# Performance work log

Hardware: AMD Instinct MI355X
Metric: run time of the kernel (lower is better)

## Reference

```python
import jax, jax.numpy as jnp
import numpy as np

P, U, B, C, S = 200000, 100000, 5000, 2000, 1000
N = P + U + B + C + S
E_PB, E_PC, E_PS, E_UP = 200000, 200000, 400000, 1000000


def setup_inputs() -> dict:
    key = jax.random.key(0)
    ks = jax.random.split(key, 21)
    d = {
        'product_x': jax.random.normal(ks[0], (P, 384), jnp.float32),
        'user_emb': jax.random.normal(ks[1], (U, 64), jnp.float32),
        'brand_emb': jax.random.normal(ks[2], (B, 64), jnp.float32),
        'cat_emb': jax.random.normal(ks[3], (C, 64), jnp.float32),
        'shop_emb': jax.random.normal(ks[4], (S, 64), jnp.float32),
        'proj_W': jax.random.normal(ks[5], (384, 64), jnp.float32) * 0.05,
        'proj_b': jax.random.normal(ks[6], (64,), jnp.float32) * 0.05,
        'c1_Wl': jax.random.normal(ks[7], (64, 64), jnp.float32) * 0.1,
        'c1_bl': jax.random.normal(ks[8], (64,), jnp.float32) * 0.1,
        'c1_Wr': jax.random.normal(ks[9], (64, 64), jnp.float32) * 0.1,
        'c2_Wl': jax.random.normal(ks[10], (64, 32), jnp.float32) * 0.1,
        'c2_bl': jax.random.normal(ks[11], (32,), jnp.float32) * 0.1,
        'c2_Wr': jax.random.normal(ks[12], (64, 32), jnp.float32) * 0.1,
        'pb_src': jax.random.randint(ks[13], (E_PB,), 0, P, jnp.int32),
        'pb_dst': jax.random.randint(ks[14], (E_PB,), 0, B, jnp.int32),
        'pc_src': jax.random.randint(ks[15], (E_PC,), 0, P, jnp.int32),
        'pc_dst': jax.random.randint(ks[16], (E_PC,), 0, C, jnp.int32),
        'ps_src': jax.random.randint(ks[17], (E_PS,), 0, P, jnp.int32),
        'ps_dst': jax.random.randint(ks[18], (E_PS,), 0, S, jnp.int32),
        'up_src': jax.random.randint(ks[19], (E_UP,), 0, U, jnp.int32),
        'up_dst': jax.random.randint(ks[20], (E_UP,), 0, P, jnp.int32),
    }
    return d


def _combined_edges(pb_src, pb_dst, pc_src, pc_dst, ps_src, ps_dst, up_src, up_dst):
    # global node id offsets: [product | user | brand | category | shop]
    off_u, off_b, off_c, off_s = P, P + U, P + U + B, P + U + B + C
    pb_d = pb_dst + off_b
    pc_d = pc_dst + off_c
    ps_d = ps_dst + off_s
    up_s = up_src + off_u
    src = jnp.concatenate([pb_src, pb_d, pc_src, pc_d, ps_src, ps_d, up_s, up_dst])
    dst = jnp.concatenate([pb_d, pb_src, pc_d, pc_src, ps_d, ps_src, up_dst, up_s])
    return src, dst


def _sage_conv(x, src, dst, Wl, bl, Wr):
    # PyG SAGEConv (mean aggr): out = lin_l(mean_{j in N(i)} x_j) + lin_r(x_i)
    msg = x[src]  # [E, d] gather
    ssum = jax.ops.segment_sum(msg, dst, num_segments=N)
    cnt = jax.ops.segment_sum(jnp.ones((src.shape[0],), x.dtype), dst, num_segments=N)
    aggr = ssum / jnp.maximum(cnt, 1.0)[:, None]
    return aggr @ Wl + bl + x @ Wr


def reference(product_x, user_emb, brand_emb, cat_emb, shop_emb,
              proj_W, proj_b, c1_Wl, c1_bl, c1_Wr, c2_Wl, c2_bl, c2_Wr,
              pb_src, pb_dst, pc_src, pc_dst, ps_src, ps_dst, up_src, up_dst):
    prod_h = jax.nn.relu(product_x @ proj_W + proj_b)
    x = jnp.concatenate([prod_h, user_emb, brand_emb, cat_emb, shop_emb], axis=0)  # [N, 64]
    src, dst = _combined_edges(pb_src, pb_dst, pc_src, pc_dst, ps_src, ps_dst, up_src, up_dst)
    x = jax.nn.relu(_sage_conv(x, src, dst, c1_Wl, c1_bl, c1_Wr))
    # dropout(p=0.2) is identity in eval mode
    x = _sage_conv(x, src, dst, c2_Wl, c2_bl, c2_Wr)  # [N, 32]
    # output_dict is just contiguous slices of x: product/user/brand/category/shop
    return x
```

## Files before the change

kernel.cpp:

```cpp
#include <hip/hip_runtime.h>

#define NP 200000
#define NU 100000
#define NBR 5000
#define NCAT 2000
#define NSH 1000
#define NN (NP + NU + NBR + NCAT + NSH)
#define OFF_U NP
#define OFF_B (NP + NU)
#define OFF_C (NP + NU + NBR)
#define OFF_S (NP + NU + NBR + NCAT)

#define NBINS 67

typedef unsigned short u16;
typedef unsigned int u32;
typedef __attribute__((ext_vector_type(8))) short short8;
typedef __attribute__((ext_vector_type(4))) float f32x4;

__device__ __forceinline__ u16 f2bf(float f) {
  union { float f; unsigned u; } v;
  v.f = f;
  unsigned r = (v.u + 0x7fffu + ((v.u >> 16) & 1u)) >> 16;
  return (u16)r;
}
__device__ __forceinline__ float uasf(u32 u) {
  union { u32 u; float f; } v;
  v.u = u;
  return v.f;
}
__device__ __forceinline__ u32 cvtpk(float lo, float hi) {
  u32 r;
  asm("v_cvt_pk_bf16_f32 %0, %1, %2" : "=v"(r) : "v"(lo), "v"(hi));
  return r;
}

__device__ __forceinline__ int bin_of(int a) {
  if (a < OFF_U) return a >> 13;
  if (a < OFF_B) return 25 + ((a - OFF_U) >> 13);
  if (a < OFF_C) return 38 + ((a - OFF_B) >> 10);
  if (a < OFF_S) return 43 + ((a - OFF_C) >> 8);
  return 51 + ((a - OFF_S) >> 6);
}
__device__ __forceinline__ void bin_range(int bin, int& n0, int& n1) {
  if (bin < 25) {
    n0 = bin << 13; n1 = min(n0 + 8192, OFF_U);
  } else if (bin < 38) {
    n0 = OFF_U + ((bin - 25) << 13); n1 = min(n0 + 8192, OFF_B);
  } else if (bin < 43) {
    n0 = OFF_B + ((bin - 38) << 10); n1 = min(n0 + 1024, OFF_C);
  } else if (bin < 51) {
    n0 = OFF_C + ((bin - 43) << 8); n1 = min(n0 + 256, OFF_S);
  } else {
    n0 = OFF_S + ((bin - 51) << 6); n1 = min(n0 + 64, NN);
  }
}

__global__ __launch_bounds__(256) void proj_mfma_kernel(
    const float* __restrict__ px, const float* __restrict__ W,
    const float* __restrict__ bias, u16* __restrict__ xb) {
  __shared__ u16 lA[2][128 * 32];
  const int t = threadIdx.x;
  const int l = t & 63;
  const int wid = t >> 6;
  const int row0 = blockIdx.x * 128;

  const int n0 = wid * 16 + (l & 15);
  const int kb = (l >> 4) * 8;
  short8 bf[12];
#pragma unroll
  for (int kt = 0; kt < 12; ++kt) {
    union { u32 p[4]; short8 s; } uu;
#pragma unroll
    for (int j = 0; j < 4; ++j) {
      const float lo = W[(size_t)(kt * 32 + kb + 2 * j) * 64 + n0];
      const float hi = W[(size_t)(kt * 32 + kb + 2 * j + 1) * 64 + n0];
      uu.p[j] = cvtpk(lo, hi);
    }
    bf[kt] = uu.s;
  }
  const float bv = bias[n0];

  f32x4 acc[8];
#pragma unroll
  for (int rt = 0; rt < 8; ++rt) {
    f32x4 z = {0.f, 0.f, 0.f, 0.f};
    acc[rt] = z;
  }

  const int fr_base = (((l & 15) * 64 + (l >> 4) * 16)) ^ ((l & 7) << 4);

  float4 sreg[4];
#pragma unroll
  for (int i = 0; i < 4; ++i) {
    const int qi = t + 256 * i;
    const int r = qi >> 3, q = qi & 7;
    const int grow = row0 + r;
    sreg[i] = (grow < NP) ? *reinterpret_cast<const float4*>(px + (size_t)grow * 384 + q * 4)
                          : make_float4(0.f, 0.f, 0.f, 0.f);
  }
#pragma unroll
  for (int i = 0; i < 4; ++i) {
    const int qi = t + 256 * i;
    const int r = qi >> 3, q = qi & 7;
    const int a16 = (((r * 64 + q * 8)) ^ ((r & 7) << 4)) >> 1;
    const u32 p0 = cvtpk(sreg[i].x, sreg[i].y);
    const u32 p1 = cvtpk(sreg[i].z, sreg[i].w);
    *reinterpret_cast<uint2*>(&lA[0][a16]) = make_uint2(p0, p1);
  }

#pragma unroll
  for (int kt = 0; kt < 12; ++kt) {
    const int cur = kt & 1;
    if (kt + 1 < 12) {
#pragma unroll
      for (int i = 0; i < 4; ++i) {
        const int qi = t + 256 * i;
        const int r = qi >> 3, q = qi & 7;
        const int grow = row0 + r;
        sreg[i] = (grow < NP)
                      ? *reinterpret_cast<const float4*>(px + (size_t)grow * 384 +
                                                         (kt + 1) * 32 + q * 4)
                      : make_float4(0.f, 0.f, 0.f, 0.f);
      }
    }
    __syncthreads();
#pragma unroll
    for (int rt = 0; rt < 8; ++rt) {
      const short8 af =
          *reinterpret_cast<const short8*>(&lA[cur][(fr_base + rt * 1024) >> 1]);
      acc[rt] = __builtin_amdgcn_mfma_f32_16x16x32_bf16(af, bf[kt], acc[rt], 0, 0, 0);
    }
    if (kt + 1 < 12) {
#pragma unroll
      for (int i = 0; i < 4; ++i) {
        const int qi = t + 256 * i;
        const int r = qi >> 3, q = qi & 7;
        const int a16 = (((r * 64 + q * 8)) ^ ((r & 7) << 4)) >> 1;
        const u32 p0 = cvtpk(sreg[i].x, sreg[i].y);
        const u32 p1 = cvtpk(sreg[i].z, sreg[i].w);
        *reinterpret_cast<uint2*>(&lA[cur ^ 1][a16]) = make_uint2(p0, p1);
      }
    }
  }

#pragma unroll
  for (int rt = 0; rt < 8; ++rt) {
#pragma unroll
    for (int r = 0; r < 4; ++r) {
      const int grow = row0 + rt * 16 + (l >> 4) * 4 + r;
      if (grow < NP)
        xb[(size_t)grow * 64 + n0] = f2bf(fmaxf(acc[rt][r] + bv, 0.f));
    }
  }
}

__global__ void cvt_emb_kernel(const float* __restrict__ ue, const float* __restrict__ be,
                               const float* __restrict__ ce, const float* __restrict__ se,
                               u16* __restrict__ xb) {
  const int i = blockIdx.x * 256 + threadIdx.x;
  const int totalQ = (NU + NBR + NCAT + NSH) * 16;
  if (i >= totalQ) return;
  const int row = i >> 4, q = i & 15;
  const float* src;
  int lrow;
  if (row < NU) {
    src = ue; lrow = row;
  } else if (row < NU + NBR) {
    src = be; lrow = row - NU;
  } else if (row < NU + NBR + NCAT) {
    src = ce; lrow = row - NU - NBR;
  } else {
    src = se; lrow = row - NU - NBR - NCAT;
  }
  const float4 v = reinterpret_cast<const float4*>(src)[(size_t)lrow * 16 + q];
  ushort4 o;
  o.x = f2bf(v.x);
  o.y = f2bf(v.y);
  o.z = f2bf(v.z);
  o.w = f2bf(v.w);
  reinterpret_cast<ushort4*>(xb + (size_t)(OFF_U + row) * 64)[q] = o;
}

__device__ __forceinline__ void decode_edge(
    int i, const int* pbs, const int* pbd, const int* pcs, const int* pcd,
    const int* pss, const int* psd, const int* ups, const int* upd,
    int nPB, int nPC, int nPS, int& a, int& b) {
  const int d = i & 1;
  int eu = i >> 1;
  int a0, b0;
  if (eu < nPB) {
    a0 = pbs[eu]; b0 = pbd[eu] + OFF_B;
  } else {
    eu -= nPB;
    if (eu < nPC) {
      a0 = pcs[eu]; b0 = pcd[eu] + OFF_C;
    } else {
      eu -= nPC;
      if (eu < nPS) {
        a0 = pss[eu]; b0 = psd[eu] + OFF_S;
      } else {
        eu -= nPS;
        a0 = ups[eu] + OFF_U; b0 = upd[eu];
      }
    }
  }
  a = d ? b0 : a0;
  b = d ? a0 : b0;
}

#define EDGE_ARGS const int* __restrict__ pbs, const int* __restrict__ pbd, \
                  const int* __restrict__ pcs, const int* __restrict__ pcd, \
                  const int* __restrict__ pss, const int* __restrict__ psd, \
                  const int* __restrict__ ups, const int* __restrict__ upd, \
                  int nPB, int nPC, int nPS, int nD
#define EDGE_PASS pbs, pbd, pcs, pcd, pss, psd, ups, upd, nPB, nPC, nPS

__global__ __launch_bounds__(256) void bin_count_kernel(EDGE_ARGS,
                                                        int* __restrict__ binCnt) {
  __shared__ int lh[NBINS];
  const int t = threadIdx.x;
  if (t < NBINS) lh[t] = 0;
  __syncthreads();
  for (int i = blockIdx.x * 256 + t; i < nD; i += gridDim.x * 256) {
    int a, b;
    decode_edge(i, EDGE_PASS, a, b);
    (void)b;
    atomicAdd(&lh[bin_of(a)], 1);
  }
  __syncthreads();
  if (t < NBINS && lh[t] > 0) atomicAdd(&binCnt[t], lh[t]);
}

__global__ void bin_scan_kernel(const int* __restrict__ binCnt, int* __restrict__ binBase,
                                int* __restrict__ gcur) {
  __shared__ int base[NBINS + 1];
  if (threadIdx.x == 0) {
    int run = 0;
    for (int b = 0; b < NBINS; ++b) {
      base[b] = run;
      run += binCnt[b];
    }
    base[NBINS] = run;
  }
  __syncthreads();
  if (threadIdx.x <= NBINS) binBase[threadIdx.x] = base[threadIdx.x];
  if (threadIdx.x < NBINS) gcur[threadIdx.x * 16] = base[threadIdx.x];
}

__global__ __launch_bounds__(256) void bin_scatter_kernel(EDGE_ARGS,
                                                          uint2* __restrict__ gbuf,
                                                          int* __restrict__ gcur) {
  __shared__ int lh[NBINS];
  __shared__ int gb[NBINS];
  __shared__ int ofs[NBINS];
  const int t = threadIdx.x;
  const int per = (nD + gridDim.x - 1) / gridDim.x;
  const int start = blockIdx.x * per;
  const int end = (start + per < nD) ? (start + per) : nD;

  if (t < NBINS) {
    lh[t] = 0;
    ofs[t] = 0;
  }
  __syncthreads();
  for (int i = start + t; i < end; i += 256) {
    int a, b;
    decode_edge(i, EDGE_PASS, a, b);
    (void)b;
    atomicAdd(&lh[bin_of(a)], 1);
  }
  __syncthreads();
  if (t < NBINS && lh[t] > 0) gb[t] = atomicAdd(&gcur[t * 16], lh[t]);
  __syncthreads();
  for (int i = start + t; i < end; i += 256) {
    int a, b;
    decode_edge(i, EDGE_PASS, a, b);
    const int bb = bin_of(a);
    const int d = atomicAdd(&ofs[bb], 1);
    gbuf[gb[bb] + d] = make_uint2((u32)a, (u32)b);
  }
}

__global__ __launch_bounds__(256) void count_nodes_kernel(
    const uint2* __restrict__ gbuf, const int* __restrict__ binBase,
    int* __restrict__ cntp) {
  __shared__ int cnt[8192];
  const int bin = blockIdx.x >> 2, s = blockIdx.x & 3;
  int n0, n1;
  bin_range(bin, n0, n1);
  const int rb = binBase[bin], re = binBase[bin + 1];
  const int len = re - rb;
  const int s0 = rb + (len * s) / 4;
  const int s1 = rb + (len * (s + 1)) / 4;
  for (int i = threadIdx.x; i < 8192; i += 256) cnt[i] = 0;
  __syncthreads();
  for (int r = s0 + threadIdx.x; r < s1; r += 256)
    atomicAdd(&cnt[(int)gbuf[r].x - n0], 1);
  __syncthreads();
  for (int n = n0 + threadIdx.x; n < n1; n += 256)
    cntp[s * NN + n] = cnt[n - n0];
}

__global__ __launch_bounds__(256) void scan1_kernel(const int* __restrict__ cntp,
                                                    int* __restrict__ blockSums, int n) {
  __shared__ int sdata[256];
  const int base = blockIdx.x * 1024;
  int s = 0;
  for (int i = threadIdx.x; i < 1024; i += 256) {
    int idx = base + i;
    if (idx < n)
      s += cntp[idx] + cntp[NN + idx] + cntp[2 * NN + idx] + cntp[3 * NN + idx];
  }
  sdata[threadIdx.x] = s;
  __syncthreads();
  for (int off = 128; off > 0; off >>= 1) {
    if (threadIdx.x < off) sdata[threadIdx.x] += sdata[threadIdx.x + off];
    __syncthreads();
  }
  if (threadIdx.x == 0) blockSums[blockIdx.x] = sdata[0];
}

__global__ __launch_bounds__(512) void scan2_kernel(int* __restrict__ blockSums, int nb) {
  __shared__ int sd[512];
  const int t = threadIdx.x;
  const int v = (t < nb) ? blockSums[t] : 0;
  sd[t] = v;
  __syncthreads();
  for (int off = 1; off < 512; off <<= 1) {
    int add = (t >= off) ? sd[t - off] : 0;
    __syncthreads();
    sd[t] += add;
    __syncthreads();
  }
  if (t < nb) blockSums[t] = sd[t] - v;
}

__global__ __launch_bounds__(256) void scan3_kernel(const int* __restrict__ cntp,
                                                    const int* __restrict__ blockSums,
                                                    int* __restrict__ rowptr, int n) {
  __shared__ int wsum[4];
  const int base = blockIdx.x * 1024;
  const int t = threadIdx.x, lane = t & 63, wid = t >> 6;
  const int idx0 = base + t * 4;
  int v[4];
#pragma unroll
  for (int j = 0; j < 4; ++j) {
    int idx = idx0 + j;
    v[j] = (idx < n)
               ? cntp[idx] + cntp[NN + idx] + cntp[2 * NN + idx] + cntp[3 * NN + idx]
               : 0;
  }
  const int s = v[0] + v[1] + v[2] + v[3];
  int incl = s;
  for (int off = 1; off < 64; off <<= 1) {
    int tt = __shfl_up(incl, off);
    if (lane >= off) incl += tt;
  }
  if (lane == 63) wsum[wid] = incl;
  __syncthreads();
  int wOff = 0;
#pragma unroll
  for (int w = 0; w < 4; ++w)
    if (w < wid) wOff += wsum[w];
  int run = blockSums[blockIdx.x] + wOff + (incl - s);
#pragma unroll
  for (int j = 0; j < 4; ++j) {
    int idx = idx0 + j;
    if (idx < n) {
      rowptr[idx] = run;
      run += v[j];
      if (idx == n - 1) rowptr[n] = run;
    }
  }
}

__global__ __launch_bounds__(256) void fill_scatter_kernel(
    const uint2* __restrict__ gbuf, const int* __restrict__ binBase,
    const int* __restrict__ rowptr, const int* __restrict__ cntp,
    int* __restrict__ eidx) {
  __shared__ int cur[8192];
  const int bin = blockIdx.x >> 2, s = blockIdx.x & 3;
  int n0, n1;
  bin_range(bin, n0, n1);
  const int rb = binBase[bin], re = binBase[bin + 1];
  const int len = re - rb;
  const int s0 = rb + (len * s) / 4;
  const int s1 = rb + (len * (s + 1)) / 4;
  for (int n = n0 + threadIdx.x; n < n1; n += 256) {
    int c = rowptr[n];
    if (s > 0) c += cntp[n];
    if (s > 1) c += cntp[NN + n];
    if (s > 2) c += cntp[2 * NN + n];
    cur[n - n0] = c;
  }
  __syncthreads();
  for (int r = s0 + threadIdx.x; r < s1; r += 256) {
    const uint2 rec = gbuf[r];
    const int p = atomicAdd(&cur[(int)rec.x - n0], 1);
    eidx[p] = (int)rec.y;
  }
}

__global__ __launch_bounds__(256) void gather_mean_kernel(
    const int* __restrict__ rowptr, const int* __restrict__ eidx,
    const uint4* __restrict__ xin, uint4* __restrict__ sout) {
  const int lane = threadIdx.x & 63;
  const int q = lane & 7;
  const int h = lane >> 3;
  const int wid0 = blockIdx.x * 4 + (threadIdx.x >> 6);
  const int nW = gridDim.x * 4;
  for (int node = wid0; node < NN; node += nW) {
    const int r0 = rowptr[node], r1 = rowptr[node + 1];
    float s0 = 0.f, s1 = 0.f, s2 = 0.f, s3 = 0.f, s4 = 0.f, s5 = 0.f, s6 = 0.f,
          s7 = 0.f;
    for (int e = r0; e < r1; e += 16) {
      const int ee0 = e + h;
      const int ee1 = e + 8 + h;
      uint4 va = make_uint4(0u, 0u, 0u, 0u);
      uint4 vb = make_uint4(0u, 0u, 0u, 0u);
      if (ee0 < r1) va = xin[(size_t)eidx[ee0] * 8 + q];
      if (ee1 < r1) vb = xin[(size_t)eidx[ee1] * 8 + q];
      s0 += uasf(va.x << 16) + uasf(vb.x << 16);
      s1 += uasf(va.x & 0xffff0000u) + uasf(vb.x & 0xffff0000u);
      s2 += uasf(va.y << 16) + uasf(vb.y << 16);
      s3 += uasf(va.y & 0xffff0000u) + uasf(vb.y & 0xffff0000u);
      s4 += uasf(va.z << 16) + uasf(vb.z << 16);
      s5 += uasf(va.z & 0xffff0000u) + uasf(vb.z & 0xffff0000u);
      s6 += uasf(va.w << 16) + uasf(vb.w << 16);
      s7 += uasf(va.w & 0xffff0000u) + uasf(vb.w & 0xffff0000u);
    }
#pragma unroll
    for (int off = 8; off < 64; off <<= 1) {
      s0 += __shfl_xor(s0, off);
      s1 += __shfl_xor(s1, off);
      s2 += __shfl_xor(s2, off);
      s3 += __shfl_xor(s3, off);
      s4 += __shfl_xor(s4, off);
      s5 += __shfl_xor(s5, off);
      s6 += __shfl_xor(s6, off);
      s7 += __shfl_xor(s7, off);
    }
    if (h == 0) {
      const int deg = r1 - r0;
      const float inv = (deg > 0) ? (1.f / (float)deg) : 1.f;
      uint4 o;
      o.x = cvtpk(s0 * inv, s1 * inv);
      o.y = cvtpk(s2 * inv, s3 * inv);
      o.z = cvtpk(s4 * inv, s5 * inv);
      o.w = cvtpk(s6 * inv, s7 * inv);
      sout[(size_t)node * 8 + q] = o;
    }
  }
}

template <int DOUT, bool RELU>
__global__ __launch_bounds__(256) void layer_gemm_kernel(
    const u32* __restrict__ S, const u32* __restrict__ X,
    const float* __restrict__ Wl, const float* __restrict__ bl,
    const float* __restrict__ Wr, void* __restrict__ outv) {
  constexpr int NC = DOUT / 4;
  constexpr int NR = 256 / NC;
  constexpr int R = 128 / NR;
  __shared__ __align__(16) u32 lS[128 * 32];
  __shared__ __align__(16) u32 lX[128 * 32];
  __shared__ __align__(16) float lWl[64 * DOUT];
  __shared__ __align__(16) float lWr[64 * DOUT];
  const int t = threadIdx.x;
  const int row0 = blockIdx.x * 128;

#pragma unroll
  for (int i = 0; i < (64 * DOUT) / 1024; ++i) {
    const int idx = i * 256 + t;
    reinterpret_cast<float4*>(lWl)[idx] = reinterpret_cast<const float4*>(Wl)[idx];
    reinterpret_cast<float4*>(lWr)[idx] = reinterpret_cast<const float4*>(Wr)[idx];
  }
#pragma unroll
  for (int i = 0; i < 4; ++i) {
    const int idx = i * 256 + t;
    const int r = idx >> 3, c = idx & 7;
    uint4 vs = make_uint4(0u, 0u, 0u, 0u), vx = vs;
    if (row0 + r < NN) {
      vs = reinterpret_cast<const uint4*>(S)[(size_t)(row0 + r) * 8 + c];
      vx = reinterpret_cast<const uint4*>(X)[(size_t)(row0 + r) * 8 + c];
    }
    reinterpret_cast<uint4*>(lS)[idx] = vs;
    reinterpret_cast<uint4*>(lX)[idx] = vx;
  }
  __syncthreads();

  const int cg = t % NC, rg = t / NC;
  const int c0 = cg * 4;
  float acc[R][4];
#pragma unroll
  for (int r = 0; r < R; ++r)
#pragma unroll
    for (int c = 0; c < 4; ++c) acc[r][c] = 0.f;

  for (int kq = 0; kq < 16; ++kq) {
    float4 wl4[4], wr4[4];
#pragma unroll
    for (int j = 0; j < 4; ++j) {
      wl4[j] = *reinterpret_cast<const float4*>(&lWl[(kq * 4 + j) * DOUT + c0]);
      wr4[j] = *reinterpret_cast<const float4*>(&lWr[(kq * 4 + j) * DOUT + c0]);
    }
#pragma unroll
    for (int r = 0; r < R; ++r) {
      const int row = rg * R + r;
      const uint2 sv = *reinterpret_cast<const uint2*>(&lS[row * 32 + kq * 2]);
      const uint2 xv = *reinterpret_cast<const uint2*>(&lX[row * 32 + kq * 2]);
      const float sf[4] = {uasf(sv.x << 16), uasf(sv.x & 0xffff0000u),
                           uasf(sv.y << 16), uasf(sv.y & 0xffff0000u)};
      const float xf[4] = {uasf(xv.x << 16), uasf(xv.x & 0xffff0000u),
                           uasf(xv.y << 16), uasf(xv.y & 0xffff0000u)};
#pragma unroll
      for (int j = 0; j < 4; ++j) {
        acc[r][0] = fmaf(sf[j], wl4[j].x, acc[r][0]);
        acc[r][1] = fmaf(sf[j], wl4[j].y, acc[r][1]);
        acc[r][2] = fmaf(sf[j], wl4[j].z, acc[r][2]);
        acc[r][3] = fmaf(sf[j], wl4[j].w, acc[r][3]);
        acc[r][0] = fmaf(xf[j], wr4[j].x, acc[r][0]);
        acc[r][1] = fmaf(xf[j], wr4[j].y, acc[r][1]);
        acc[r][2] = fmaf(xf[j], wr4[j].z, acc[r][2]);
        acc[r][3] = fmaf(xf[j], wr4[j].w, acc[r][3]);
      }
    }
  }

  const float b0 = bl[c0 + 0], b1 = bl[c0 + 1], b2 = bl[c0 + 2], b3 = bl[c0 + 3];
#pragma unroll
  for (int r = 0; r < R; ++r) {
    const int grow = row0 + rg * R + r;
    if (grow < NN) {
      float o0 = acc[r][0] + b0, o1 = acc[r][1] + b1, o2 = acc[r][2] + b2, o3 = acc[r][3] + b3;
      if (RELU) {
        o0 = fmaxf(o0, 0.f); o1 = fmaxf(o1, 0.f); o2 = fmaxf(o2, 0.f); o3 = fmaxf(o3, 0.f);
      }
      if (DOUT == 64) {
        ushort4 o;
        o.x = f2bf(o0); o.y = f2bf(o1); o.z = f2bf(o2); o.w = f2bf(o3);
        *reinterpret_cast<ushort4*>((u16*)outv + (size_t)grow * 64 + c0) = o;
      } else {
        float4 o = make_float4(o0, o1, o2, o3);
        *reinterpret_cast<float4*>((float*)outv + (size_t)grow * 32 + c0) = o;
      }
    }
  }
}

extern "C" void kernel_launch(void* const* d_in, const int* in_sizes, int n_in,
                              void* d_out, int out_size, void* d_ws, size_t ws_size,
                              hipStream_t stream) {
  const float* product_x = (const float*)d_in[0];
  const float* user_emb = (const float*)d_in[1];
  const float* brand_emb = (const float*)d_in[2];
  const float* cat_emb = (const float*)d_in[3];
  const float* shop_emb = (const float*)d_in[4];
  const float* proj_W = (const float*)d_in[5];
  const float* proj_b = (const float*)d_in[6];
  const float* c1_Wl = (const float*)d_in[7];
  const float* c1_bl = (const float*)d_in[8];
  const float* c1_Wr = (const float*)d_in[9];
  const float* c2_Wl = (const float*)d_in[10];
  const float* c2_bl = (const float*)d_in[11];
  const float* c2_Wr = (const float*)d_in[12];
  const int* pb_src = (const int*)d_in[13];
  const int* pb_dst = (const int*)d_in[14];
  const int* pc_src = (const int*)d_in[15];
  const int* pc_dst = (const int*)d_in[16];
  const int* ps_src = (const int*)d_in[17];
  const int* ps_dst = (const int*)d_in[18];
  const int* up_src = (const int*)d_in[19];
  const int* up_dst = (const int*)d_in[20];
  const int nPB = in_sizes[13], nPC = in_sizes[15], nPS = in_sizes[17], nUP = in_sizes[19];
  const int nE = nPB + nPC + nPS + nUP;
  const int nD = 2 * nE;

  u16* xb = (u16*)d_ws;
  u16* out1 = xb + (size_t)NN * 64;
  u16* sbuf = out1 + (size_t)NN * 64;
  int* eidx = (int*)(sbuf + (size_t)NN * 64);
  int* rowptr = eidx + nD;
  int* blockSums = rowptr + (NN + 1);
  int* binCnt = blockSums + 512;
  int* binBase = binCnt + 128;
  int* gcur = binBase + 128;
  uint2* gbuf = (uint2*)sbuf;
  int* cntp = (int*)out1;

  hipMemsetAsync(binCnt, 0, 128 * sizeof(int), stream);

  bin_count_kernel<<<512, 256, 0, stream>>>(pb_src, pb_dst, pc_src, pc_dst, ps_src, ps_dst,
                                            up_src, up_dst, nPB, nPC, nPS, nD, binCnt);
  bin_scan_kernel<<<1, 128, 0, stream>>>(binCnt, binBase, gcur);
  bin_scatter_kernel<<<512, 256, 0, stream>>>(pb_src, pb_dst, pc_src, pc_dst, ps_src, ps_dst,
                                              up_src, up_dst, nPB, nPC, nPS, nD, gbuf, gcur);
  count_nodes_kernel<<<NBINS * 4, 256, 0, stream>>>(gbuf, binBase, cntp);

  const int nb = (NN + 1023) / 1024;
  scan1_kernel<<<nb, 256, 0, stream>>>(cntp, blockSums, NN);
  scan2_kernel<<<1, 512, 0, stream>>>(blockSums, nb);
  scan3_kernel<<<nb, 256, 0, stream>>>(cntp, blockSums, rowptr, NN);

  fill_scatter_kernel<<<NBINS * 4, 256, 0, stream>>>(gbuf, binBase, rowptr, cntp, eidx);

  proj_mfma_kernel<<<(NP + 127) / 128, 256, 0, stream>>>(product_x, proj_W, proj_b, xb);
  cvt_emb_kernel<<<((NU + NBR + NCAT + NSH) * 16 + 255) / 256, 256, 0, stream>>>(
      user_emb, brand_emb, cat_emb, shop_emb, xb);

  gather_mean_kernel<<<4096, 256, 0, stream>>>(rowptr, eidx, (const uint4*)xb,
                                               (uint4*)sbuf);
  layer_gemm_kernel<64, true><<<(NN + 127) / 128, 256, 0, stream>>>(
      (const u32*)sbuf, (const u32*)xb, c1_Wl, c1_bl, c1_Wr, out1);
  gather_mean_kernel<<<4096, 256, 0, stream>>>(rowptr, eidx, (const uint4*)out1,
                                               (uint4*)sbuf);
  layer_gemm_kernel<32, false><<<(NN + 127) / 128, 256, 0, stream>>>(
      (const u32*)sbuf, (const u32*)out1, c2_Wl, c2_bl, c2_Wr, d_out);
}
```

Baseline: 608.9 us.

## Fuse neighbor mean gather with layer GEMM using bf16 MFMA in shared memory

Combines the gather-mean aggregation and the per-layer linear transform into one kernel per SAGE layer. Each block aggregates 128 nodes into swizzled LDS and runs the Wl/Wr product with 16x16x32 bf16 MFMA instead of scalar FP32 FMAs. This removes the write and re-read of the aggregated buffer and two launches. The trade-offs are lower parallelism in the gather phase (a fixed 128 nodes per block rather than a grid-stride loop), weights rounded to bf16, and scalar 2-byte or 4-byte output stores.

After: 2.157 ms. 3.54x slower.

```diff
diff --git a/kernel.cpp b/kernel.cpp
--- a/kernel.cpp
+++ b/kernel.cpp
@@ -402,16 +402,62 @@
   }
 }
 
-__global__ __launch_bounds__(256) void gather_mean_kernel(
+template <int DOUT, bool RELU>
+__global__ __launch_bounds__(256) void fused_layer_kernel(
     const int* __restrict__ rowptr, const int* __restrict__ eidx,
-    const uint4* __restrict__ xin, uint4* __restrict__ sout) {
-  const int lane = threadIdx.x & 63;
-  const int q = lane & 7;
-  const int h = lane >> 3;
-  const int wid0 = blockIdx.x * 4 + (threadIdx.x >> 6);
-  const int nW = gridDim.x * 4;
-  for (int node = wid0; node < NN; node += nW) {
-    const int r0 = rowptr[node], r1 = rowptr[node + 1];
+    const uint4* __restrict__ xin ,
+    const float* __restrict__ Wl, const float* __restrict__ bl,
+    const float* __restrict__ Wr, void* __restrict__ outv) {
+  __shared__ u16 lS[128 * 64];
+  __shared__ u16 lX[128 * 64];
+  const int t = threadIdx.x;
+  const int l = t & 63;
+  const int wid = t >> 6;
+  const int row0 = blockIdx.x * 128;
+
+  uint4 xreg[4];
+#pragma unroll
+  for (int i = 0; i < 4; ++i) {
+    const int idx = i * 256 + t;
+    const int r = idx >> 3, qq = idx & 7;
+    xreg[i] = (row0 + r < NN) ? xin[(size_t)(row0 + r) * 8 + qq]
+                              : make_uint4(0u, 0u, 0u, 0u);
+  }
+
+  const int n0 = (DOUT == 64 ? wid * 16 : (wid & 1) * 16) + (l & 15);
+  const int kb = (l >> 4) * 8;
+  short8 bfl[2], bfr[2];
+#pragma unroll
+  for (int kt = 0; kt < 2; ++kt) {
+    union { u32 p[4]; short8 s; } ul, ur;
+#pragma unroll
+    for (int j = 0; j < 4; ++j) {
+      const int k = kt * 32 + kb + 2 * j;
+      ul.p[j] = cvtpk(Wl[(size_t)k * DOUT + n0], Wl[(size_t)(k + 1) * DOUT + n0]);
+      ur.p[j] = cvtpk(Wr[(size_t)k * DOUT + n0], Wr[(size_t)(k + 1) * DOUT + n0]);
+    }
+    bfl[kt] = ul.s;
+    bfr[kt] = ur.s;
+  }
+  const float bv = bl[n0];
+
+#pragma unroll
+  for (int i = 0; i < 4; ++i) {
+    const int idx = i * 256 + t;
+    const int r = idx >> 3, qq = idx & 7;
+    *reinterpret_cast<uint4*>(
+        reinterpret_cast<char*>(lX) + ((r * 128 + qq * 16) ^ ((r & 7) << 4))) = xreg[i];
+  }
+
+  const int q = l & 7;
+  const int h = l >> 3;
+  for (int ln = wid * 32; ln < wid * 32 + 32; ++ln) {
+    const int node = row0 + ln;
+    int r0 = 0, r1 = 0;
+    if (node < NN) {
+      r0 = rowptr[node];
+      r1 = rowptr[node + 1];
+    }
     float s0 = 0.f, s1 = 0.f, s2 = 0.f, s3 = 0.f, s4 = 0.f, s5 = 0.f, s6 = 0.f,
           s7 = 0.f;
     for (int e = r0; e < r1; e += 16) {
@@ -449,100 +495,47 @@
       o.y = cvtpk(s2 * inv, s3 * inv);
       o.z = cvtpk(s4 * inv, s5 * inv);
       o.w = cvtpk(s6 * inv, s7 * inv);
-      sout[(size_t)node * 8 + q] = o;
-    }
-  }
-}
-
-template <int DOUT, bool RELU>
-__global__ __launch_bounds__(256) void layer_gemm_kernel(
-    const u32* __restrict__ S, const u32* __restrict__ X,
-    const float* __restrict__ Wl, const float* __restrict__ bl,
-    const float* __restrict__ Wr, void* __restrict__ outv) {
-  constexpr int NC = DOUT / 4;
-  constexpr int NR = 256 / NC;
-  constexpr int R = 128 / NR;
-  __shared__ __align__(16) u32 lS[128 * 32];
-  __shared__ __align__(16) u32 lX[128 * 32];
-  __shared__ __align__(16) float lWl[64 * DOUT];
-  __shared__ __align__(16) float lWr[64 * DOUT];
-  const int t = threadIdx.x;
-  const int row0 = blockIdx.x * 128;
-
-#pragma unroll
-  for (int i = 0; i < (64 * DOUT) / 1024; ++i) {
-    const int idx = i * 256 + t;
-    reinterpret_cast<float4*>(lWl)[idx] = reinterpret_cast<const float4*>(Wl)[idx];
-    reinterpret_cast<float4*>(lWr)[idx] = reinterpret_cast<const float4*>(Wr)[idx];
-  }
-#pragma unroll
-  for (int i = 0; i < 4; ++i) {
-    const int idx = i * 256 + t;
-    const int r = idx >> 3, c = idx & 7;
-    uint4 vs = make_uint4(0u, 0u, 0u, 0u), vx = vs;
-    if (row0 + r < NN) {
-      vs = reinterpret_cast<const uint4*>(S)[(size_t)(row0 + r) * 8 + c];
-      vx = reinterpret_cast<const uint4*>(X)[(size_t)(row0 + r) * 8 + c];
-    }
-    reinterpret_cast<uint4*>(lS)[idx] = vs;
-    reinterpret_cast<uint4*>(lX)[idx] = vx;
-  }
-  __syncthreads();
-
-  const int cg = t % NC, rg = t / NC;
-  const int c0 = cg * 4;
-  float acc[R][4];
-#pragma unroll
-  for (int r = 0; r < R; ++r)
-#pragma unroll
-    for (int c = 0; c < 4; ++c) acc[r][c] = 0.f;
-
-  for (int kq = 0; kq < 16; ++kq) {
-    float4 wl4[4], wr4[4];
-#pragma unroll
-    for (int j = 0; j < 4; ++j) {
-      wl4[j] = *reinterpret_cast<const float4*>(&lWl[(kq * 4 + j) * DOUT + c0]);
-      wr4[j] = *reinterpret_cast<const float4*>(&lWr[(kq * 4 + j) * DOUT + c0]);
-    }
-#pragma unroll
-    for (int r = 0; r < R; ++r) {
-      const int row = rg * R + r;
-      const uint2 sv = *reinterpret_cast<const uint2*>(&lS[row * 32 + kq * 2]);
-      const uint2 xv = *reinterpret_cast<const uint2*>(&lX[row * 32 + kq * 2]);
-      const float sf[4] = {uasf(sv.x << 16), uasf(sv.x & 0xffff0000u),
-                           uasf(sv.y << 16), uasf(sv.y & 0xffff0000u)};
-      const float xf[4] = {uasf(xv.x << 16), uasf(xv.x & 0xffff0000u),
-                           uasf(xv.y << 16), uasf(xv.y & 0xffff0000u)};
-#pragma unroll
-      for (int j = 0; j < 4; ++j) {
-        acc[r][0] = fmaf(sf[j], wl4[j].x, acc[r][0]);
-        acc[r][1] = fmaf(sf[j], wl4[j].y, acc[r][1]);
-        acc[r][2] = fmaf(sf[j], wl4[j].z, acc[r][2]);
-        acc[r][3] = fmaf(sf[j], wl4[j].w, acc[r][3]);
-        acc[r][0] = fmaf(xf[j], wr4[j].x, acc[r][0]);
-        acc[r][1] = fmaf(xf[j], wr4[j].y, acc[r][1]);
-        acc[r][2] = fmaf(xf[j], wr4[j].z, acc[r][2]);
-        acc[r][3] = fmaf(xf[j], wr4[j].w, acc[r][3]);
-      }
-    }
-  }
-
-  const float b0 = bl[c0 + 0], b1 = bl[c0 + 1], b2 = bl[c0 + 2], b3 = bl[c0 + 3];
-#pragma unroll
-  for (int r = 0; r < R; ++r) {
-    const int grow = row0 + rg * R + r;
-    if (grow < NN) {
-      float o0 = acc[r][0] + b0, o1 = acc[r][1] + b1, o2 = acc[r][2] + b2, o3 = acc[r][3] + b3;
-      if (RELU) {
-        o0 = fmaxf(o0, 0.f); o1 = fmaxf(o1, 0.f); o2 = fmaxf(o2, 0.f); o3 = fmaxf(o3, 0.f);
-      }
-      if (DOUT == 64) {
-        ushort4 o;
-        o.x = f2bf(o0); o.y = f2bf(o1); o.z = f2bf(o2); o.w = f2bf(o3);
-        *reinterpret_cast<ushort4*>((u16*)outv + (size_t)grow * 64 + c0) = o;
-      } else {
-        float4 o = make_float4(o0, o1, o2, o3);
-        *reinterpret_cast<float4*>((float*)outv + (size_t)grow * 32 + c0) = o;
+      *reinterpret_cast<uint4*>(
+          reinterpret_cast<char*>(lS) + ((ln * 128 + q * 16) ^ ((ln & 7) << 4))) = o;
+    }
+  }
+  __syncthreads();
+
+  constexpr int NRT = (DOUT == 64) ? 8 : 4;
+  const int rbase = (DOUT == 64) ? 0 : (wid >> 1) * 64;
+  f32x4 acc[NRT];
+#pragma unroll
+  for (int rt = 0; rt < NRT; ++rt) {
+    f32x4 z = {0.f, 0.f, 0.f, 0.f};
+    acc[rt] = z;
+  }
+#pragma unroll
+  for (int kt = 0; kt < 2; ++kt) {
+#pragma unroll
+    for (int rt = 0; rt < NRT; ++rt) {
+      const int row = rbase + rt * 16 + (l & 15);
+      const int boff = (row * 128 + (kt * 4 + (l >> 4)) * 16) ^ ((row & 7) << 4);
+      const short8 aS =
+          *reinterpret_cast<const short8*>(reinterpret_cast<const char*>(lS) + boff);
+      acc[rt] = __builtin_amdgcn_mfma_f32_16x16x32_bf16(aS, bfl[kt], acc[rt], 0, 0, 0);
+      const short8 aX =
+          *reinterpret_cast<const short8*>(reinterpret_cast<const char*>(lX) + boff);
+      acc[rt] = __builtin_amdgcn_mfma_f32_16x16x32_bf16(aX, bfr[kt], acc[rt], 0, 0, 0);
+    }
+  }
+
+#pragma unroll
+  for (int rt = 0; rt < NRT; ++rt) {
+#pragma unroll
+    for (int r = 0; r < 4; ++r) {
+      const int grow = row0 + rbase + rt * 16 + (l >> 4) * 4 + r;
+      if (grow < NN) {
+        float o = acc[rt][r] + bv;
+        if (RELU) o = fmaxf(o, 0.f);
+        if (DOUT == 64)
+          ((u16*)outv)[(size_t)grow * 64 + n0] = f2bf(o);
+        else
+          ((float*)outv)[(size_t)grow * 32 + n0] = o;
       }
     }
   }
@@ -578,14 +571,14 @@
 
   u16* xb = (u16*)d_ws;
   u16* out1 = xb + (size_t)NN * 64;
-  u16* sbuf = out1 + (size_t)NN * 64;
-  int* eidx = (int*)(sbuf + (size_t)NN * 64);
+  u16* scratch = out1 + (size_t)NN * 64;
+  int* eidx = (int*)(scratch + (size_t)NN * 64);
   int* rowptr = eidx + nD;
   int* blockSums = rowptr + (NN + 1);
   int* binCnt = blockSums + 512;
   int* binBase = binCnt + 128;
   int* gcur = binBase + 128;
-  uint2* gbuf = (uint2*)sbuf;
+  uint2* gbuf = (uint2*)scratch;
   int* cntp = (int*)out1;
 
   hipMemsetAsync(binCnt, 0, 128 * sizeof(int), stream);
@@ -608,12 +601,9 @@
   cvt_emb_kernel<<<((NU + NBR + NCAT + NSH) * 16 + 255) / 256, 256, 0, stream>>>(
       user_emb, brand_emb, cat_emb, shop_emb, xb);
 
-  gather_mean_kernel<<<4096, 256, 0, stream>>>(rowptr, eidx, (const uint4*)xb,
-                                               (uint4*)sbuf);
-  layer_gemm_kernel<64, true><<<(NN + 127) / 128, 256, 0, stream>>>(
-      (const u32*)sbuf, (const u32*)xb, c1_Wl, c1_bl, c1_Wr, out1);
-  gather_mean_kernel<<<4096, 256, 0, stream>>>(rowptr, eidx, (const uint4*)out1,
-                                               (uint4*)sbuf);
-  layer_gemm_kernel<32, false><<<(NN + 127) / 128, 256, 0, stream>>>(
-      (const u32*)sbuf, (const u32*)out1, c2_Wl, c2_bl, c2_Wr, d_out);
-}
+  const int nBlk = (NN + 127) / 128;
+  fused_layer_kernel<64, true><<<nBlk, 256, 0, stream>>>(
+      rowptr, eidx, (const uint4*)xb, c1_Wl, c1_bl, c1_Wr, out1);
+  fused_layer_kernel<32, false><<<nBlk, 256, 0, stream>>>(
+      rowptr, eidx, (const uint4*)out1, c2_Wl, c2_bl, c2_Wr, d_out);
+}
```
